# Kernel tuning notes

Measured on AMD Instinct MI355X. Metric: run time of the kernel, lower is better.

## Reference

```python
import jax, jax.numpy as jnp
import numpy as np

EPS = 1e-5
B, N, D, H = 4, 2048, 1024, 16
DH = D // H


def ln(x, w, b):
    m = x.mean(-1, keepdims=True)
    v = ((x - m) ** 2).mean(-1, keepdims=True)
    return (x - m) * jax.lax.rsqrt(v + EPS) * w + b


def setup_inputs() -> dict:
    key = jax.random.key(0)
    ks = jax.random.split(key, 12)
    s = D ** -0.5
    x = jax.random.normal(ks[0], (B, N, D), jnp.float32)
    attention_mask = jax.random.randint(ks[1], (B, N), 0, 2) > 0
    return {
        "x": x,
        "attention_mask": attention_mask,
        "norm_w": jnp.ones((D,), jnp.float32),
        "norm_b": jnp.zeros((D,), jnp.float32),
        "qn_w": jnp.ones((DH,), jnp.float32),
        "qn_b": jnp.zeros((DH,), jnp.float32),
        "kn_w": jnp.ones((DH,), jnp.float32),
        "kn_b": jnp.zeros((DH,), jnp.float32),
        "Wq": jax.random.normal(ks[2], (D, D), jnp.float32) * s,
        "bq": jnp.zeros((D,), jnp.float32),
        "Wk": jax.random.normal(ks[3], (D, D), jnp.float32) * s,
        "bk": jnp.zeros((D,), jnp.float32),
        "Wv": jax.random.normal(ks[4], (D, D), jnp.float32) * s,
        "bv": jnp.zeros((D,), jnp.float32),
        "Wo": jax.random.normal(ks[5], (D, D), jnp.float32) * s,
    }


def reference(x, attention_mask, norm_w, norm_b, qn_w, qn_b, kn_w, kn_b,
              Wq, bq, Wk, bk, Wv, bv, Wo):
    b, n, d = x.shape
    scale = DH ** -0.5
    xn = ln(x, norm_w, norm_b)                       # pre-norm; context = xn (self-attn)
    q = (xn @ Wq.T + bq).reshape(b, n, H, DH).transpose(0, 2, 1, 3)  # b h n d
    k = (xn @ Wk.T + bk).reshape(b, n, H, DH).transpose(0, 2, 1, 3)
    v = (xn @ Wv.T + bv).reshape(b, n, H, DH).transpose(0, 2, 1, 3)
    q = ln(q, qn_w, qn_b) * scale                    # QK layernorm over head dim
    k = ln(k, kn_w, kn_b)
    sim = jnp.einsum('bhid,bhjd->bhij', q, k)        # full [b,h,n,n] scores
    sim = jnp.where(attention_mask[:, None, None, :], sim, -jnp.inf)
    attn = jax.nn.softmax(sim, axis=-1)
    out = jnp.einsum('bhij,bhjd->bhid', attn, v)
    out = out.transpose(0, 2, 1, 3).reshape(b, n, d)
    return out @ Wo.T
```

## Files before the change

### kernel.cpp

```cpp
#include <hip/hip_runtime.h>
#include <hip/hip_bf16.h>
#include <cstdint>

typedef unsigned short u16;
typedef unsigned int   u32;
typedef __attribute__((ext_vector_type(8))) short short8;
typedef __attribute__((ext_vector_type(4))) float f32x4;
typedef __attribute__((ext_vector_type(4))) u32  u32x4;
typedef __attribute__((ext_vector_type(2))) u32  u32x2;

#define DEV static __device__ __forceinline__

DEV float bf2f(u16 u){ u32 t = ((u32)u) << 16; float f; __builtin_memcpy(&f, &t, 4); return f; }
DEV u16 f2bf(float f){ u32 t; __builtin_memcpy(&t, &f, 4); return (u16)((t + 0x7fffu + ((t >> 16) & 1u)) >> 16); }

#if __has_builtin(__builtin_amdgcn_exp2f)
DEV float fast_exp2(float x){ return __builtin_amdgcn_exp2f(x); }
#else
DEV float fast_exp2(float x){ return exp2f(x); }
#endif

DEV u32 pack_trunc(float x, float y){
    u32 tx, ty; __builtin_memcpy(&tx, &x, 4); __builtin_memcpy(&ty, &y, 4);
#if __has_builtin(__builtin_amdgcn_perm)
    return __builtin_amdgcn_perm(ty, tx, 0x07060302);
#else
    return (tx >> 16) | (ty & 0xFFFF0000u);
#endif
}

DEV void gload_lds16(const void* g, void* l) {
    __builtin_amdgcn_global_load_lds((__attribute__((address_space(1))) void*)(g),
                                     (__attribute__((address_space(3))) void*)(l), 16, 0, 0);
}

__global__ __launch_bounds__(256) void detect_mode(const u16* __restrict__ x, int* __restrict__ mode)
{
    __shared__ int red[4];
    const int tid = threadIdx.x;
    int crazy = 0;
    for (int i = tid; i < 1024; i += 256) {
        u16 v = x[2 * i];
        int e = (v >> 7) & 0xFF;
        if (e >= 0x9F || (e > 0 && e <= 0x5F)) crazy++;
    }
    #pragma unroll
    for (int off = 1; off < 64; off <<= 1) crazy += __shfl_xor(crazy, off, 64);
    if ((tid & 63) == 0) red[tid >> 6] = crazy;
    __syncthreads();
    if (tid == 0) *mode = (red[0] + red[1] + red[2] + red[3] > 128) ? 1 : 0;
}

struct SrcPtrs { const void* p[13]; };

__global__ __launch_bounds__(256) void convert_params(SrcPtrs sp, u16* __restrict__ ws,
                                                      const int* __restrict__ mode)
{
    const bool f = (*mode != 0);
    u16* cW = ws + 33554432;
    u16* cV = ws + 37748736;
    if (blockIdx.x < 16384) {
        const int i = blockIdx.x * 256 + threadIdx.x;
        const int t = i >> 20, off = i & 1048575;
        const void* src = (t == 0) ? sp.p[6] : (t == 1) ? sp.p[8] : (t == 2) ? sp.p[10] : sp.p[12];
        cW[i] = f ? f2bf(((const float*)src)[off]) : ((const u16*)src)[off];
    } else {
        const int j = (blockIdx.x - 16384) * 256 + threadIdx.x;
        if (j >= 5376) return;
        const void* src; int off;
        if      (j < 1024) { src = sp.p[0];  off = j; }
        else if (j < 2048) { src = sp.p[1];  off = j - 1024; }
        else if (j < 3072) { src = sp.p[7];  off = j - 2048; }
        else if (j < 4096) { src = sp.p[9];  off = j - 3072; }
        else if (j < 5120) { src = sp.p[11]; off = j - 4096; }
        else { int m = j - 5120; src = sp.p[2 + (m >> 6)]; off = m & 63; }
        cV[j] = f ? f2bf(((const float*)src)[off]) : ((const u16*)src)[off];
    }
}

__global__ __launch_bounds__(256) void ln_kernel(const void* __restrict__ x,
                                                 const u16* __restrict__ w,
                                                 const u16* __restrict__ b,
                                                 u16* __restrict__ xn,
                                                 const int* __restrict__ mode)
{
    const int row = blockIdx.x;
    const int tid = threadIdx.x;
    const int wv = tid >> 6, lane = tid & 63;

    float v0, v1, v2, v3;
    if (*mode) {
        f32x4 r = *((const f32x4*)((const float*)x + row * 1024) + tid);
        v0 = r[0]; v1 = r[1]; v2 = r[2]; v3 = r[3];
    } else {
        u32x2 raw = *(const u32x2*)((const u16*)x + row * 1024 + tid * 4);
        v0 = bf2f((u16)(raw.x & 0xffff)); v1 = bf2f((u16)(raw.x >> 16));
        v2 = bf2f((u16)(raw.y & 0xffff)); v3 = bf2f((u16)(raw.y >> 16));
    }
    float s  = v0 + v1 + v2 + v3;
    float sq = v0*v0 + v1*v1 + v2*v2 + v3*v3;
    #pragma unroll
    for (int off = 1; off < 64; off <<= 1) {
        s  += __shfl_xor(s,  off, 64);
        sq += __shfl_xor(sq, off, 64);
    }
    __shared__ float red[8];
    if (lane == 0) { red[wv] = s; red[4 + wv] = sq; }
    __syncthreads();
    float ts = red[0] + red[1] + red[2] + red[3];
    float tq = red[4] + red[5] + red[6] + red[7];
    float mean = ts * (1.0f / 1024.0f);
    float var  = tq * (1.0f / 1024.0f) - mean * mean;
    float rs   = rsqrtf(var + 1e-5f);

    float y0 = (v0 - mean) * rs * bf2f(w[tid*4+0]) + bf2f(b[tid*4+0]);
    float y1 = (v1 - mean) * rs * bf2f(w[tid*4+1]) + bf2f(b[tid*4+1]);
    float y2 = (v2 - mean) * rs * bf2f(w[tid*4+2]) + bf2f(b[tid*4+2]);
    float y3 = (v3 - mean) * rs * bf2f(w[tid*4+3]) + bf2f(b[tid*4+3]);
    u32x2 out;
    out.x = (u32)f2bf(y0) | ((u32)f2bf(y1) << 16);
    out.y = (u32)f2bf(y2) | ((u32)f2bf(y3) << 16);
    *(u32x2*)(xn + row * 1024 + tid * 4) = out;
}

__global__ __launch_bounds__(256, 4) void gemm128(const u16* __restrict__ A,
                                                  const u16* __restrict__ W,
                                                  const u16* __restrict__ bias,
                                                  void* __restrict__ out0,
                                                  u16* __restrict__ vt,
                                                  const u16* __restrict__ qnw, const u16* __restrict__ qnb,
                                                  const u16* __restrict__ knw, const u16* __restrict__ knb,
                                                  const int* __restrict__ mode,
                                                  int epi, int N)
{
    __shared__ u16 As[128 * 64];
    __shared__ u16 Bs[128 * 64];
    const int tid = threadIdx.x;
    const int m0 = blockIdx.x * 128, n0 = blockIdx.y * 128;
    const int wv = tid >> 6, lane = tid & 63, quad = lane >> 4, l16 = lane & 15;
    const int wm = wv & 1, wn = wv >> 1;

    f32x4 acc[4][4] = {};

    const int srow = tid >> 3;
    const int scol = (((tid & 7) - (srow & 7)) & 7) * 8;
    const u16* Ap = A + (size_t)(m0 + srow) * 1024 + scol;
    const u16* Wp = W + (size_t)(n0 + srow) * 1024 + scol;

    const int swz0 = ((quad     + l16) & 7) * 8;
    const int swz1 = ((quad + 4 + l16) & 7) * 8;

    for (int k0 = 0; k0 < 1024; k0 += 64) {
        #pragma unroll
        for (int i = 0; i < 4; i++)
            gload_lds16(Ap + k0 + (size_t)i * 32 * 1024, &As[i * 2048 + wv * 512]);
        #pragma unroll
        for (int i = 0; i < 4; i++)
            gload_lds16(Wp + k0 + (size_t)i * 32 * 1024, &Bs[i * 2048 + wv * 512]);
        __syncthreads();
        #pragma unroll
        for (int kh = 0; kh < 2; kh++) {
            const int sw = kh ? swz1 : swz0;
            short8 af[4], bf[4];
            #pragma unroll
            for (int mi = 0; mi < 4; mi++)
                af[mi] = *(const short8*)&As[(wm * 64 + mi * 16 + l16) * 64 + sw];
            #pragma unroll
            for (int ni = 0; ni < 4; ni++)
                bf[ni] = *(const short8*)&Bs[(wn * 64 + ni * 16 + l16) * 64 + sw];
            #pragma unroll
            for (int mi = 0; mi < 4; mi++)
                #pragma unroll
                for (int ni = 0; ni < 4; ni++)
                    acc[mi][ni] = __builtin_amdgcn_mfma_f32_16x16x32_bf16(af[mi], bf[ni], acc[mi][ni], 0, 0, 0);
        }
        __syncthreads();
    }

    if (epi == 1) {
        const int colbase = n0 + wn * 64;
        if (colbase < 2048) {
            const bool isK = colbase >= 1024;
            const u16* lw = isK ? knw : qnw;
            const u16* lb = isK ? knb : qnb;
            const float scale = isK ? 1.0f : 0.18033688011112042f;
            float lnw[4], lnb2[4], bv[4];
            #pragma unroll
            for (int ni = 0; ni < 4; ni++) {
                const int dh = ni * 16 + l16;
                lnw[ni] = bf2f(lw[dh]); lnb2[ni] = bf2f(lb[dh]); bv[ni] = bf2f(bias[colbase + dh]);
            }
            u16* qk = (u16*)out0;
            #pragma unroll
            for (int mi = 0; mi < 4; mi++) {
                #pragma unroll
                for (int r = 0; r < 4; r++) {
                    float v[4];
                    float s = 0.0f, sq = 0.0f;
                    #pragma unroll
                    for (int ni = 0; ni < 4; ni++) {
                        v[ni] = acc[mi][ni][r] + bv[ni];
                        s += v[ni]; sq += v[ni] * v[ni];
                    }
                    #pragma unroll
                    for (int off = 1; off < 16; off <<= 1) {
                        s  += __shfl_xor(s,  off, 64);
                        sq += __shfl_xor(sq, off, 64);
                    }
                    const float mean = s * (1.0f / 64.0f);
                    const float var  = sq * (1.0f / 64.0f) - mean * mean;
                    const float rs   = rsqrtf(var + 1e-5f);
                    const int row = m0 + wm * 64 + mi * 16 + quad * 4 + r;
                    #pragma unroll
                    for (int ni = 0; ni < 4; ni++)
                        qk[(size_t)row * 2048 + colbase + ni * 16 + l16] =
                            f2bf(((v[ni] - mean) * rs * lnw[ni] + lnb2[ni]) * scale);
                }
            }
        } else {
            const int cp0 = colbase - 2048;
            #pragma unroll
            for (int ni = 0; ni < 4; ni++) {
                const int cp = cp0 + ni * 16 + l16;
                const int h = cp >> 6, dh = cp & 63;
                const float bvv = bf2f(bias[2048 + cp]);
                #pragma unroll
                for (int mi = 0; mi < 4; mi++) {
                    const int row0 = m0 + wm * 64 + mi * 16 + quad * 4;
                    const int bb = row0 >> 11, nn = row0 & 2047;
                    u32x2 pk;
                    pk.x = (u32)f2bf(acc[mi][ni][0] + bvv) | ((u32)f2bf(acc[mi][ni][1] + bvv) << 16);
                    pk.y = (u32)f2bf(acc[mi][ni][2] + bvv) | ((u32)f2bf(acc[mi][ni][3] + bvv) << 16);
                    *(u32x2*)&vt[(size_t)(((bb * 16 + h) * 64) + dh) * 2048 + nn] = pk;
                }
            }
        }
    } else {
        const bool f32o = (*mode != 0);
        #pragma unroll
        for (int ni = 0; ni < 4; ni++) {
            const int col = n0 + wn * 64 + ni * 16 + l16;
            #pragma unroll
            for (int mi = 0; mi < 4; mi++) {
                const int row0 = m0 + wm * 64 + mi * 16 + quad * 4;
                #pragma unroll
                for (int r = 0; r < 4; r++) {
                    const float val = acc[mi][ni][r];
                    if (f32o) ((float*)out0)[(size_t)(row0 + r) * 1024 + col] = val;
                    else      ((u16*)out0)[(size_t)(row0 + r) * 1024 + col]  = f2bf(val);
                }
            }
        }
    }
}

__global__ __launch_bounds__(256, 4) void attn(const u16* __restrict__ qk, const u16* __restrict__ vt,
                                               const int* __restrict__ mask, u16* __restrict__ ctx)
{
    __shared__ __align__(16) float maskf[2048];
    __shared__ __align__(16) u16 Ks[64 * 64];
    __shared__ __align__(16) u16 Vs[64 * 64];
    __shared__ __align__(16) u16 Ps[128 * 64];

    const int bh = blockIdx.y, b = bh >> 4, h = bh & 15;
    const int i0 = blockIdx.x * 128;
    const int tid = threadIdx.x, wv = tid >> 6, lane = tid & 63, quad = lane >> 4, l16 = lane & 15;

    for (int idx = tid; idx < 2048; idx += 256)
        maskf[idx] = mask[b * 2048 + idx] ? -12.0f : -1e9f;

    const u16* qbase = qk + (size_t)(b * 2048) * 2048 + h * 64;
    const u16* kbase = qbase + 1024;
    const u16* vbase = vt + (size_t)(bh * 64) * 2048;

    short8 qf[2][2];
    #pragma unroll
    for (int g = 0; g < 2; g++) {
        const int iw = i0 + wv * 32 + g * 16 + l16;
        qf[g][0] = *(const short8*)(qbase + (size_t)iw * 2048 + quad * 8);
        qf[g][1] = *(const short8*)(qbase + (size_t)iw * 2048 + 32 + quad * 8);
    }

    f32x4 O[2][4] = {};
    float l_lane[2] = {0.0f, 0.0f};

    const int sr = lane >> 3, ss = lane & 7;
    const int sck = ((ss - sr) & 7) * 8;
    const u16* kp0 = kbase + (size_t)(wv * 16 +      sr) * 2048 + sck;
    const u16* kp1 = kbase + (size_t)(wv * 16 + 8  + sr) * 2048 + sck;
    const u16* vp0 = vbase + (size_t)(wv * 16 +      sr) * 2048 + sck;
    const u16* vp1 = vbase + (size_t)(wv * 16 + 8  + sr) * 2048 + sck;

    const int swz0 = ((quad     + l16) & 7) * 8;
    const int swz1 = ((quad + 4 + l16) & 7) * 8;
    const u16* kb0 = &Ks[l16 * 64 + swz0];
    const u16* kb1 = &Ks[l16 * 64 + swz1];
    const u16* vb0 = &Vs[l16 * 64 + swz0];
    const u16* vb1 = &Vs[l16 * 64 + swz1];
    u16* pw = &Ps[(wv * 16 + l16) * 64];

    for (int j0 = 0; j0 < 2048; j0 += 64) {
        gload_lds16(kp0, &Ks[(wv * 16    ) * 64]);
        gload_lds16(kp1, &Ks[(wv * 16 + 8) * 64]);
        gload_lds16(vp0, &Vs[(wv * 16    ) * 64]);
        gload_lds16(vp1, &Vs[(wv * 16 + 8) * 64]);
        kp0 += 64 * 2048; kp1 += 64 * 2048; vp0 += 64; vp1 += 64;
        __syncthreads();

        f32x4 sfr[2][4];
        #pragma unroll
        for (int sub = 0; sub < 4; sub++) {
            short8 kf0 = *(const short8*)(kb0 + sub * 1024);
            short8 kf1 = *(const short8*)(kb1 + sub * 1024);
            f32x4 mrow = *(const f32x4*)&maskf[j0 + sub * 16 + quad * 4];
            #pragma unroll
            for (int g = 0; g < 2; g++) {
                f32x4 sz = mrow;
                sz = __builtin_amdgcn_mfma_f32_16x16x32_bf16(kf0, qf[g][0], sz, 0, 0, 0);
                sz = __builtin_amdgcn_mfma_f32_16x16x32_bf16(kf1, qf[g][1], sz, 0, 0, 0);
                sfr[g][sub] = sz;
            }
        }

        #pragma unroll
        for (int g = 0; g < 2; g++) {
            float lp = 0.0f;
            #pragma unroll
            for (int sub = 0; sub < 4; sub++)
                #pragma unroll
                for (int r = 0; r < 4; r++) {
                    float e = fast_exp2(sfr[g][sub][r]);
                    sfr[g][sub][r] = e;
                    lp += e;
                }
            l_lane[g] += lp;
            #pragma unroll
            for (int sub = 0; sub < 4; sub++) {
                u32x2 pk;
                pk.x = pack_trunc(sfr[g][sub][0], sfr[g][sub][1]);
                pk.y = pack_trunc(sfr[g][sub][2], sfr[g][sub][3]);
                *(u32x2*)(pw + g * 4096 + ((sub * 2 + (quad >> 1) + l16) & 7) * 8 + (quad & 1) * 4) = pk;
            }
        }

        short8 pf[2][2];
        #pragma unroll
        for (int g = 0; g < 2; g++) {
            pf[g][0] = *(const short8*)(pw + g * 4096 + swz0);
            pf[g][1] = *(const short8*)(pw + g * 4096 + swz1);
        }
        #pragma unroll
        for (int dht = 0; dht < 4; dht++) {
            short8 vf0 = *(const short8*)(vb0 + dht * 1024);
            short8 vf1 = *(const short8*)(vb1 + dht * 1024);
            #pragma unroll
            for (int g = 0; g < 2; g++) {
                O[g][dht] = __builtin_amdgcn_mfma_f32_16x16x32_bf16(vf0, pf[g][0], O[g][dht], 0, 0, 0);
                O[g][dht] = __builtin_amdgcn_mfma_f32_16x16x32_bf16(vf1, pf[g][1], O[g][dht], 0, 0, 0);
            }
        }
        __syncthreads();
    }

    #pragma unroll
    for (int g = 0; g < 2; g++) {
        float l = l_lane[g];
        l += __shfl_xor(l, 16, 64);
        l += __shfl_xor(l, 32, 64);
        const float inv = l > 0.0f ? 1.0f / l : 0.0f;
        const int iw = i0 + wv * 32 + g * 16 + l16;
        u16* cb = ctx + (size_t)(b * 2048 + iw) * 1024 + h * 64;
        #pragma unroll
        for (int dht = 0; dht < 4; dht++) {
            u32x2 pk;
            pk.x = (u32)f2bf(O[g][dht][0] * inv) | ((u32)f2bf(O[g][dht][1] * inv) << 16);
            pk.y = (u32)f2bf(O[g][dht][2] * inv) | ((u32)f2bf(O[g][dht][3] * inv) << 16);
            *(u32x2*)(cb + dht * 16 + quad * 4) = pk;
        }
    }
}

extern "C" void kernel_launch(void* const* d_in, const int* in_sizes, int n_in,
                              void* d_out, int out_size, void* d_ws, size_t ws_size,
                              hipStream_t stream)
{
    const int* mask = (const int*)d_in[1];

    u16* ws = (u16*)d_ws;
    u16* xn  = ws;
    u16* qkb = ws + 8388608;
    u16* vtb = ws + 25165824;
    u16* ctx = xn;
    u16* cW  = ws + 33554432;
    u16* cV  = ws + 37748736;
    int* mode = (int*)(ws + 37754176);

    detect_mode<<<dim3(1), dim3(256), 0, stream>>>((const u16*)d_in[0], mode);

    SrcPtrs sp;
    for (int i = 0; i < 13; i++) sp.p[i] = d_in[i + 2];
    convert_params<<<dim3(16405), dim3(256), 0, stream>>>(sp, ws, mode);

    ln_kernel<<<dim3(8192), dim3(256), 0, stream>>>(d_in[0], cV + 0, cV + 1024, xn, mode);

    gemm128<<<dim3(64, 24), dim3(256), 0, stream>>>(xn, cW, cV + 2048, qkb, vtb,
                                                    cV + 5120, cV + 5184, cV + 5248, cV + 5312,
                                                    mode, 1, 3072);

    attn<<<dim3(16, 64), dim3(256), 0, stream>>>(qkb, vtb, mask, ctx);

    gemm128<<<dim3(64, 8), dim3(256), 0, stream>>>(ctx, cW + 3145728, nullptr, d_out, nullptr,
                                                   nullptr, nullptr, nullptr, nullptr,
                                                   mode, 2, 1024);
}
```

Baseline: 302.7 us.

## Double-buffer K/V tiles and pass P through permlane swaps instead of LDS

```diff
diff --git a/kernel.cpp b/kernel.cpp
--- a/kernel.cpp
+++ b/kernel.cpp
@@ -32,6 +32,19 @@
 DEV void gload_lds16(const void* g, void* l) {
     __builtin_amdgcn_global_load_lds((__attribute__((address_space(1))) void*)(g),
                                      (__attribute__((address_space(3))) void*)(l), 16, 0, 0);
+}
+
+DEV short8 xchg_quads(u32 a0, u32 a1, u32 b0, u32 b1)
+{
+    u32 x0 = a0, y0 = b0;
+    asm("v_permlane32_swap_b32 %0, %1" : "+v"(x0), "+v"(y0));
+    asm("v_permlane16_swap_b32 %0, %1" : "+v"(x0), "+v"(y0));
+    u32 x1 = a1, y1 = b1;
+    asm("v_permlane32_swap_b32 %0, %1" : "+v"(x1), "+v"(y1));
+    asm("v_permlane16_swap_b32 %0, %1" : "+v"(x1), "+v"(y1));
+    union { u32 w[4]; short8 v; } u;
+    u.w[0] = x0; u.w[1] = x1; u.w[2] = y0; u.w[3] = y1;
+    return u.v;
 }
 
 __global__ __launch_bounds__(256) void detect_mode(const u16* __restrict__ x, int* __restrict__ mode)
@@ -254,13 +267,73 @@
     }
 }
 
+#define ATTN_STAGE(BUF) do { \
+    gload_lds16(kp0, &Ks[BUF][wv * 1024]); \
+    gload_lds16(kp1, &Ks[BUF][wv * 1024 + 512]); \
+    gload_lds16(vp0, &Vs[BUF][wv * 1024]); \
+    gload_lds16(vp1, &Vs[BUF][wv * 1024 + 512]); \
+    kp0 += 64 * 2048; kp1 += 64 * 2048; vp0 += 64; vp1 += 64; } while (0)
+
+#define ATTN_BODY(CUR, NXT, J0, DO_STAGE, DO_BAR) do { \
+    if (DO_STAGE) ATTN_STAGE(NXT); \
+    f32x4 sfr[2][4]; \
+    _Pragma("unroll") \
+    for (int sub = 0; sub < 4; sub++) { \
+        short8 kf0 = *(const short8*)&Ks[CUR][krow + swz0 + sub * 1024]; \
+        short8 kf1 = *(const short8*)&Ks[CUR][krow + swz1 + sub * 1024]; \
+        f32x4 mrow = *(const f32x4*)&maskf[(J0) + sub * 16 + quad * 4]; \
+        _Pragma("unroll") \
+        for (int g = 0; g < 2; g++) { \
+            f32x4 sz = mrow; \
+            sz = __builtin_amdgcn_mfma_f32_16x16x32_bf16(kf0, qf[g][0], sz, 0, 0, 0); \
+            sz = __builtin_amdgcn_mfma_f32_16x16x32_bf16(kf1, qf[g][1], sz, 0, 0, 0); \
+            sfr[g][sub] = sz; \
+        } \
+    } \
+    short8 pf[2][2]; \
+    _Pragma("unroll") \
+    for (int g = 0; g < 2; g++) { \
+        float lp = 0.0f; \
+        _Pragma("unroll") \
+        for (int sub = 0; sub < 4; sub++) \
+            _Pragma("unroll") \
+            for (int r = 0; r < 4; r++) { \
+                float e = fast_exp2(sfr[g][sub][r]); \
+                sfr[g][sub][r] = e; lp += e; \
+            } \
+        l_lane[g] += lp; \
+        u32 W00 = pack_trunc(sfr[g][0][0], sfr[g][0][1]); \
+        u32 W01 = pack_trunc(sfr[g][0][2], sfr[g][0][3]); \
+        u32 W10 = pack_trunc(sfr[g][1][0], sfr[g][1][1]); \
+        u32 W11 = pack_trunc(sfr[g][1][2], sfr[g][1][3]); \
+        u32 W20 = pack_trunc(sfr[g][2][0], sfr[g][2][1]); \
+        u32 W21 = pack_trunc(sfr[g][2][2], sfr[g][2][3]); \
+        u32 W30 = pack_trunc(sfr[g][3][0], sfr[g][3][1]); \
+        u32 W31 = pack_trunc(sfr[g][3][2], sfr[g][3][3]); \
+        pf[g][0] = xchg_quads(W00, W01, W10, W11); \
+        pf[g][1] = xchg_quads(W20, W21, W30, W31); \
+    } \
+    _Pragma("unroll") \
+    for (int dht = 0; dht < 4; dht++) { \
+        short8 vf0 = *(const short8*)&Vs[CUR][krow + swz0 + dht * 1024]; \
+        short8 vf1 = *(const short8*)&Vs[CUR][krow + swz1 + dht * 1024]; \
+        _Pragma("unroll") \
+        for (int g = 0; g < 2; g++) { \
+            O[g][dht] = __builtin_amdgcn_mfma_f32_16x16x32_bf16(vf0, pf[g][0], O[g][dht], 0, 0, 0); \
+            O[g][dht] = __builtin_amdgcn_mfma_f32_16x16x32_bf16(vf1, pf[g][1], O[g][dht], 0, 0, 0); \
+        } \
+    } \
+    if (DO_BAR) { \
+        asm volatile("s_waitcnt vmcnt(0)" ::: "memory"); \
+        __builtin_amdgcn_s_barrier(); \
+    } } while (0)
+
 __global__ __launch_bounds__(256, 4) void attn(const u16* __restrict__ qk, const u16* __restrict__ vt,
                                                const int* __restrict__ mask, u16* __restrict__ ctx)
 {
     __shared__ __align__(16) float maskf[2048];
-    __shared__ __align__(16) u16 Ks[64 * 64];
-    __shared__ __align__(16) u16 Vs[64 * 64];
-    __shared__ __align__(16) u16 Ps[128 * 64];
+    __shared__ __align__(16) u16 Ks[2][64 * 64];
+    __shared__ __align__(16) u16 Vs[2][64 * 64];
 
     const int bh = blockIdx.y, b = bh >> 4, h = bh & 15;
     const int i0 = blockIdx.x * 128;
@@ -293,73 +366,16 @@
 
     const int swz0 = ((quad     + l16) & 7) * 8;
     const int swz1 = ((quad + 4 + l16) & 7) * 8;
-    const u16* kb0 = &Ks[l16 * 64 + swz0];
-    const u16* kb1 = &Ks[l16 * 64 + swz1];
-    const u16* vb0 = &Vs[l16 * 64 + swz0];
-    const u16* vb1 = &Vs[l16 * 64 + swz1];
-    u16* pw = &Ps[(wv * 16 + l16) * 64];
-
-    for (int j0 = 0; j0 < 2048; j0 += 64) {
-        gload_lds16(kp0, &Ks[(wv * 16    ) * 64]);
-        gload_lds16(kp1, &Ks[(wv * 16 + 8) * 64]);
-        gload_lds16(vp0, &Vs[(wv * 16    ) * 64]);
-        gload_lds16(vp1, &Vs[(wv * 16 + 8) * 64]);
-        kp0 += 64 * 2048; kp1 += 64 * 2048; vp0 += 64; vp1 += 64;
-        __syncthreads();
-
-        f32x4 sfr[2][4];
-        #pragma unroll
-        for (int sub = 0; sub < 4; sub++) {
-            short8 kf0 = *(const short8*)(kb0 + sub * 1024);
-            short8 kf1 = *(const short8*)(kb1 + sub * 1024);
-            f32x4 mrow = *(const f32x4*)&maskf[j0 + sub * 16 + quad * 4];
-            #pragma unroll
-            for (int g = 0; g < 2; g++) {
-                f32x4 sz = mrow;
-                sz = __builtin_amdgcn_mfma_f32_16x16x32_bf16(kf0, qf[g][0], sz, 0, 0, 0);
-                sz = __builtin_amdgcn_mfma_f32_16x16x32_bf16(kf1, qf[g][1], sz, 0, 0, 0);
-                sfr[g][sub] = sz;
-            }
-        }
-
-        #pragma unroll
-        for (int g = 0; g < 2; g++) {
-            float lp = 0.0f;
-            #pragma unroll
-            for (int sub = 0; sub < 4; sub++)
-                #pragma unroll
-                for (int r = 0; r < 4; r++) {
-                    float e = fast_exp2(sfr[g][sub][r]);
-                    sfr[g][sub][r] = e;
-                    lp += e;
-                }
-            l_lane[g] += lp;
-            #pragma unroll
-            for (int sub = 0; sub < 4; sub++) {
-                u32x2 pk;
-                pk.x = pack_trunc(sfr[g][sub][0], sfr[g][sub][1]);
-                pk.y = pack_trunc(sfr[g][sub][2], sfr[g][sub][3]);
-                *(u32x2*)(pw + g * 4096 + ((sub * 2 + (quad >> 1) + l16) & 7) * 8 + (quad & 1) * 4) = pk;
-            }
-        }
-
-        short8 pf[2][2];
-        #pragma unroll
-        for (int g = 0; g < 2; g++) {
-            pf[g][0] = *(const short8*)(pw + g * 4096 + swz0);
-            pf[g][1] = *(const short8*)(pw + g * 4096 + swz1);
-        }
-        #pragma unroll
-        for (int dht = 0; dht < 4; dht++) {
-            short8 vf0 = *(const short8*)(vb0 + dht * 1024);
-            short8 vf1 = *(const short8*)(vb1 + dht * 1024);
-            #pragma unroll
-            for (int g = 0; g < 2; g++) {
-                O[g][dht] = __builtin_amdgcn_mfma_f32_16x16x32_bf16(vf0, pf[g][0], O[g][dht], 0, 0, 0);
-                O[g][dht] = __builtin_amdgcn_mfma_f32_16x16x32_bf16(vf1, pf[g][1], O[g][dht], 0, 0, 0);
-            }
-        }
-        __syncthreads();
+    const int krow = l16 * 64;
+
+    ATTN_STAGE(0);
+    asm volatile("s_waitcnt vmcnt(0) lgkmcnt(0)" ::: "memory");
+    __builtin_amdgcn_s_barrier();
+
+    for (int j0 = 0; j0 < 2048; j0 += 128) {
+        ATTN_BODY(0, 1, j0, true, true);
+        const bool more = (j0 + 128) < 2048;
+        ATTN_BODY(1, 0, j0 + 64, more, more);
     }
 
     #pragma unroll
```

Result: no change. 297.8 us (-1.6%).
